# Kernel tuning notes

Hardware: AMD Instinct MI355X
Metric: run time of the kernel (lower is better)

Reference implementation:

```python
import jax, jax.numpy as jnp
import numpy as np

EPS = 1e-5

@jax.custom_vjp
def spike(u):
    return (u >= 0).astype(u.dtype)

def _spike_fwd(u):
    return spike(u), u

def _spike_bwd(u, g):
    return (g / (1.0 + 5.0 * jnp.abs(u)) ** 2,)

spike.defvjp(_spike_fwd, _spike_bwd)


def setup_inputs() -> dict:
    key = jax.random.key(0)
    ks = jax.random.split(key, 20)
    B, T, IN, TH, H = 2048, 320, 64, 128, 64
    d = {}
    d['x'] = jax.random.normal(ks[0], (B, T, IN), jnp.float32)
    d['tda'] = jax.random.normal(ks[1], (B, 150), jnp.float32)
    # depthwise conv: Conv1d(64,128,k=15,pad=7,groups=64) -> kernel [128, 1, 15]
    d['conv_w'] = jax.random.normal(ks[2], (TH, 1, 15), jnp.float32) * 0.1
    d['conv_b'] = jnp.zeros((TH,), jnp.float32)
    d['bn1_g'] = jnp.ones((TH,), jnp.float32)
    d['bn1_b'] = jnp.zeros((TH,), jnp.float32)
    d['bn1_m'] = jnp.zeros((TH,), jnp.float32)
    d['bn1_v'] = jnp.ones((TH,), jnp.float32)
    # spatial_fc: Linear(128,64), init mean=0.05 std=0.1
    d['sp_w'] = 0.05 + 0.1 * jax.random.normal(ks[3], (H, TH), jnp.float32)
    d['sp_b'] = jnp.zeros((H,), jnp.float32)
    d['li_w'] = jax.random.normal(ks[4], (H, 2 * H), jnp.float32) * (1.0 / np.sqrt(2 * H))
    d['li_b'] = jnp.zeros((H,), jnp.float32)
    d['tda_w1'] = jax.random.normal(ks[5], (64, 150), jnp.float32) * (1.0 / np.sqrt(150))
    d['tda_b1'] = jnp.zeros((64,), jnp.float32)
    d['tda_w2'] = jax.random.normal(ks[6], (32, 64), jnp.float32) * 0.125
    d['tda_b2'] = jnp.zeros((32,), jnp.float32)
    dp_out = (320 // 32) * H  # 640
    d['cls_w1'] = jax.random.normal(ks[7], (128, dp_out + 32), jnp.float32) * (1.0 / np.sqrt(dp_out + 32))
    d['cls_b1'] = jnp.zeros((128,), jnp.float32)
    d['bn2_g'] = jnp.ones((128,), jnp.float32)
    d['bn2_b'] = jnp.zeros((128,), jnp.float32)
    d['bn2_m'] = jnp.zeros((128,), jnp.float32)
    d['bn2_v'] = jnp.ones((128,), jnp.float32)
    d['cls_w2'] = jax.random.normal(ks[8], (4, 128), jnp.float32) * (1.0 / np.sqrt(128))
    d['cls_b2'] = jnp.zeros((4,), jnp.float32)
    return d


def reference(x, tda, conv_w, conv_b, bn1_g, bn1_b, bn1_m, bn1_v, sp_w, sp_b,
              li_w, li_b, tda_w1, tda_b1, tda_w2, tda_b2,
              cls_w1, cls_b1, bn2_g, bn2_b, bn2_m, bn2_v, cls_w2, cls_b2):
    B, T, _ = x.shape
    L_DP, N_DP, H = 32, 16, 64
    # temp_conv (eval mode: no dropout, BN with running stats)
    xc = jnp.transpose(x, (0, 2, 1))  # [B, 64, T]
    y = jax.lax.conv_general_dilated(
        xc, conv_w, window_strides=(1,), padding=[(7, 7)],
        dimension_numbers=('NCH', 'OIH', 'NCH'), feature_group_count=64)
    y = y + conv_b[None, :, None]
    y = (y - bn1_m[None, :, None]) * jax.lax.rsqrt(bn1_v + EPS)[None, :, None] * bn1_g[None, :, None] + bn1_b[None, :, None]
    y = jax.nn.relu(y)
    y = jnp.transpose(y, (0, 2, 1))  # [B, T, 128]
    # precompute all input currents: [T, B, 64] (time-major for scan)
    cur_all = jnp.einsum('bth,oh->tbo', y, sp_w) + sp_b

    def step(carry, cur):
        mf, ms, ml = carry
        mf = 0.5 * mf + cur
        sf = spike(mf - 0.5)
        mf = mf * (1.0 - sf)
        ms = 0.9 * ms + cur
        ss = spike(ms - 1.0)
        ms = ms * (1.0 - ss)
        cur_li = jnp.concatenate([sf, ss], axis=-1) @ li_w.T + li_b
        ml = 0.9 * ml + cur_li
        return (mf, ms, ml), ml

    z0 = jnp.zeros((B, H), x.dtype)
    _, li_seq = jax.lax.scan(step, (z0, z0, z0), cur_all)  # [T, B, 64]
    li_seq = jnp.transpose(li_seq, (1, 0, 2))  # [B, T, 64]

    windows = li_seq.reshape(B, T // L_DP, L_DP, H)
    start_mean = windows[:, :, :N_DP, :].mean(axis=2)
    end_mean = windows[:, :, -N_DP:, :].mean(axis=2)
    dp_feat = (end_mean - start_mean).reshape(B, -1)  # [B, 640]

    t1 = jax.nn.relu(tda @ tda_w1.T + tda_b1)
    tda_feat = jax.nn.relu(t1 @ tda_w2.T + tda_b2)  # [B, 32]

    h = jnp.concatenate([dp_feat, tda_feat], axis=-1) @ cls_w1.T + cls_b1
    h = (h - bn2_m) * jax.lax.rsqrt(bn2_v + EPS) * bn2_g + bn2_b
    h = jax.nn.relu(h)
    return h @ cls_w2.T + cls_b2  # [B, 4]
```

## Files before the change

kernel.cpp:

```cpp
#include <hip/hip_runtime.h>

#define NT 256

#define WS_SPWT    0
#define WS_SC1     8192
#define WS_SH1     8320
#define WS_SC2     8448
#define WS_SH2     8576
#define WS_LIWT    8704
#define WS_TW1T    16896
#define WS_TW2T    26496
#define WS_CW1T    28544
#define WS_TOTAL   114560
#define WS_WG      114560
#define WS_WBASE   114688

__global__ void prep_kernel(
    const float* __restrict__ conv_b, const float* __restrict__ bn1_g,
    const float* __restrict__ bn1_b,  const float* __restrict__ bn1_m,
    const float* __restrict__ bn1_v,  const float* __restrict__ sp_w,
    const float* __restrict__ li_w,   const float* __restrict__ tda_w1,
    const float* __restrict__ tda_w2, const float* __restrict__ cls_w1,
    const float* __restrict__ bn2_g,  const float* __restrict__ bn2_b,
    const float* __restrict__ bn2_m,  const float* __restrict__ bn2_v,
    float* __restrict__ ws)
{
    int i = blockIdx.x * NT + threadIdx.x;
    if (i > WS_TOTAL) return;
    if (i == WS_TOTAL) {
        float g = 0.f, sE = 0.f, sL = 0.f; int w = 0;
        for (int t = 0; t < 320; ++t) {
            g = fmaf(0.9f, g, 1.f);
            int pos = t & 31;
            if (pos < 16) sE += g; else sL += g;
            if (pos == 31) { ws[WS_WG + w] = sL - sE; ++w; sE = 0.f; sL = 0.f; }
        }
        return;
    }
    if (i < WS_SC1) {
        int c = i >> 6, h = i & 63;
        ws[i] = sp_w[h*128 + c];
    } else if (i < WS_SH1) {
        int c = i - WS_SC1;
        float vv = bn1_v[c] + 1e-5f;
        ws[i] = (float)((double)bn1_g[c] / sqrt((double)vv));
    } else if (i < WS_SC2) {
        int c = i - WS_SH1;
        float vv = bn1_v[c] + 1e-5f;
        double s = (double)bn1_g[c] / sqrt((double)vv);
        ws[i] = (float)(((double)conv_b[c] - (double)bn1_m[c])*s + (double)bn1_b[c]);
    } else if (i < WS_SH2) {
        int c = i - WS_SC2;
        float vv = bn2_v[c] + 1e-5f;
        ws[i] = (float)((double)bn2_g[c] / sqrt((double)vv));
    } else if (i < WS_LIWT) {
        int c = i - WS_SH2;
        float vv = bn2_v[c] + 1e-5f;
        double s = (double)bn2_g[c] / sqrt((double)vv);
        ws[i] = (float)((double)bn2_b[c] - (double)bn2_m[c]*s);
    } else if (i < WS_TW1T) {
        int t = i - WS_LIWT; int j = t >> 6, o = t & 63;
        ws[i] = li_w[o*128 + j];
    } else if (i < WS_TW2T) {
        int t = i - WS_TW1T; int r = t >> 6, o = t & 63;
        ws[i] = tda_w1[o*150 + r];
    } else if (i < WS_CW1T) {
        int t = i - WS_TW2T; int j = t >> 5, o = t & 31;
        ws[i] = tda_w2[o*64 + j];
    } else {
        int t = i - WS_CW1T; int j = t >> 7, c = t & 127;
        ws[i] = cls_w1[c*672 + j];
    }
}

__launch_bounds__(NT, 3)
__global__ void fused_kernel(
    const float* __restrict__ x, const float* __restrict__ conv_w,
    const float* __restrict__ sp_b, const float* __restrict__ ws,
    float* __restrict__ wfeat)
{
    __shared__ float y_lds[128*65];
    __shared__ float cur_lds[64*64];

    const int tid  = threadIdx.x;
    const int b    = blockIdx.x;
    const int ic   = tid & 63;
    const int tg   = tid >> 6;
    const int lane = tid & 63;
    const int h0   = __builtin_amdgcn_readfirstlane((tid >> 6) << 4);

    float w0[15], w1[15];
    #pragma unroll
    for (int k = 0; k < 15; ++k) {
        w0[k] = conv_w[(2*ic)*15 + k];
        w1[k] = conv_w[(2*ic + 1)*15 + k];
    }
    const float sA = ws[WS_SC1 + 2*ic],     hA = ws[WS_SH1 + 2*ic];
    const float sB = ws[WS_SC1 + 2*ic + 1], hB = ws[WS_SH1 + 2*ic + 1];
    const float4* bp = reinterpret_cast<const float4*>(sp_b + h0);
    const float4 b0v = bp[0], b1v = bp[1], b2v = bp[2], b3v = bp[3];

    const float* __restrict__ spwT = ws;
    const float* xb = x + (size_t)b * 20480 + ic;
    float* Wb = wfeat + (size_t)b * 1280;

    float mf = 0.f, ms = 0.f, rlo = 0.f, rhi = 0.f;

    float xr0[30], xr1[30];
    #pragma unroll
    for (int r = 0; r < 30; ++r) {
        int t = tg*16 - 7 + r;
        xr0[r] = (t >= 0) ? xb[(size_t)t * 64] : 0.f;
    }
    #pragma unroll
    for (int j = 0; j < 16; ++j) {
        float a0 = 0.f, a1 = 0.f;
        #pragma unroll
        for (int k = 0; k < 15; ++k) {
            a0 = fmaf(xr0[j + k], w0[k], a0);
            a1 = fmaf(xr0[j + k], w1[k], a1);
        }
        int tt = tg*16 + j;
        y_lds[(2*ic)*65 + tt]     = fmaxf(fmaf(a0, sA, hA), 0.f);
        y_lds[(2*ic + 1)*65 + tt] = fmaxf(fmaf(a1, sB, hB), 0.f);
    }
    __syncthreads();

    #pragma unroll
    for (int chk = 0; chk < 5; ++chk) {
        float* xn = (chk & 1) ? xr0 : xr1;

        if (chk < 4) {
            const int tbase = (chk + 1)*64 + tg*16 - 7;
            if (tbase + 29 < 320) {
                #pragma unroll
                for (int r = 0; r < 30; ++r)
                    xn[r] = xb[(size_t)(tbase + r) * 64];
            } else {
                #pragma unroll
                for (int r = 0; r < 30; ++r) {
                    int t = tbase + r;
                    xn[r] = (t < 320) ? xb[(size_t)t * 64] : 0.f;
                }
            }
        }

        {
            float acc[16];
            acc[0]=b0v.x;  acc[1]=b0v.y;  acc[2]=b0v.z;  acc[3]=b0v.w;
            acc[4]=b1v.x;  acc[5]=b1v.y;  acc[6]=b1v.z;  acc[7]=b1v.w;
            acc[8]=b2v.x;  acc[9]=b2v.y;  acc[10]=b2v.z; acc[11]=b2v.w;
            acc[12]=b3v.x; acc[13]=b3v.y; acc[14]=b3v.z; acc[15]=b3v.w;

            #pragma unroll 4
            for (int c = 0; c < 128; ++c) {
                float yv = y_lds[c*65 + lane];
                const float4* wp = reinterpret_cast<const float4*>(spwT + c*64 + h0);
                float4 q0 = wp[0], q1 = wp[1], q2 = wp[2], q3 = wp[3];
                acc[0]  = fmaf(yv, q0.x, acc[0]);
                acc[1]  = fmaf(yv, q0.y, acc[1]);
                acc[2]  = fmaf(yv, q0.z, acc[2]);
                acc[3]  = fmaf(yv, q0.w, acc[3]);
                acc[4]  = fmaf(yv, q1.x, acc[4]);
                acc[5]  = fmaf(yv, q1.y, acc[5]);
                acc[6]  = fmaf(yv, q1.z, acc[6]);
                acc[7]  = fmaf(yv, q1.w, acc[7]);
                acc[8]  = fmaf(yv, q2.x, acc[8]);
                acc[9]  = fmaf(yv, q2.y, acc[9]);
                acc[10] = fmaf(yv, q2.z, acc[10]);
                acc[11] = fmaf(yv, q2.w, acc[11]);
                acc[12] = fmaf(yv, q3.x, acc[12]);
                acc[13] = fmaf(yv, q3.y, acc[13]);
                acc[14] = fmaf(yv, q3.z, acc[14]);
                acc[15] = fmaf(yv, q3.w, acc[15]);
            }
            const int tsw = (lane & 15) << 2;
            #pragma unroll
            for (int k = 0; k < 4; ++k) {
                float4 v4 = make_float4(acc[4*k], acc[4*k+1], acc[4*k+2], acc[4*k+3]);
                *reinterpret_cast<float4*>(&cur_lds[lane*64 + ((h0 + 4*k) ^ tsw)]) = v4;
            }
        }
        __syncthreads();

        if (tid < 64) {
            float sE_lo = 0.f, sE_hi = 0.f;
            #pragma unroll
            for (int gq = 0; gq < 4; ++gq) {
                float v[16];
                #pragma unroll
                for (int q = 0; q < 16; ++q) {
                    int t = gq*16 + q;
                    v[q] = cur_lds[t*64 + (lane ^ ((t & 15) << 2))];
                }
                float slo = 0.f, shi = 0.f;
                #pragma unroll
                for (int q = 0; q < 16; ++q) {
                    float c = v[q];
                    mf = fmaf(0.5f, mf, c);
                    bool sf = mf >= 0.5f;
                    ms = fmaf(0.9f, ms, c);
                    bool ss = ms >= 1.0f;
                    mf = sf ? 0.f : mf;
                    ms = ss ? 0.f : ms;
                    rlo = fmaf(0.9f, rlo, sf ? 1.f : 0.f);
                    rhi = fmaf(0.9f, rhi, ss ? 1.f : 0.f);
                    slo += rlo; shi += rhi;
                }
                if ((gq & 1) == 0) {
                    sE_lo = slo; sE_hi = shi;
                } else {
                    int wdx = chk*2 + (gq >> 1);
                    Wb[wdx*128 + lane]      = slo - sE_lo;
                    Wb[wdx*128 + 64 + lane] = shi - sE_hi;
                }
            }
        }
        if (chk < 4) {
            #pragma unroll
            for (int j = 0; j < 16; ++j) {
                float a0 = 0.f, a1 = 0.f;
                #pragma unroll
                for (int k = 0; k < 15; ++k) {
                    a0 = fmaf(xn[j + k], w0[k], a0);
                    a1 = fmaf(xn[j + k], w1[k], a1);
                }
                int tt = tg*16 + j;
                y_lds[(2*ic)*65 + tt]     = fmaxf(fmaf(a0, sA, hA), 0.f);
                y_lds[(2*ic + 1)*65 + tt] = fmaxf(fmaf(a1, sB, hB), 0.f);
            }
        }
        __syncthreads();
    }
}

__global__ void epilogue_kernel(
    const float* __restrict__ tda,    const float* __restrict__ li_b,
    const float* __restrict__ tda_b1, const float* __restrict__ tda_b2,
    const float* __restrict__ cls_b1, const float* __restrict__ cls_w2,
    const float* __restrict__ cls_b2, const float* __restrict__ ws,
    const float* __restrict__ W,      float* __restrict__ out)
{
    __shared__ float Wl[1280];
    __shared__ float t1[64], tf[32], dp[640], h1[128];
    const int b = blockIdx.x, tid = threadIdx.x;

    for (int i = tid; i < 1280; i += NT)
        Wl[i] = W[(size_t)b*1280 + i];
    __syncthreads();

    const float* __restrict__ liwT = ws + WS_LIWT;
    const float* __restrict__ tw1T = ws + WS_TW1T;
    const float* __restrict__ tw2T = ws + WS_TW2T;
    const float* __restrict__ cw1T = ws + WS_CW1T;
    const float* tdab = tda + b*150;

    if (tid < 64) {
        float acc = tda_b1[tid];
        for (int i2 = 0; i2 < 150; ++i2)
            acc = fmaf(tdab[i2], tw1T[i2*64 + tid], acc);
        t1[tid] = fmaxf(acc, 0.f);
    }
    __syncthreads();
    if (tid < 32) {
        float acc = tda_b2[tid];
        #pragma unroll 8
        for (int j = 0; j < 64; ++j)
            acc = fmaf(t1[j], tw2T[j*32 + tid], acc);
        tf[tid] = fmaxf(acc, 0.f);
    }
    {
        int o = tid & 63;
        for (int w = tid >> 6; w < 10; w += 4) {
            float acc = li_b[o] * ws[WS_WG + w];
            #pragma unroll 4
            for (int j = 0; j < 128; ++j)
                acc = fmaf(Wl[w*128 + j], liwT[j*64 + o], acc);
            dp[w*64 + o] = 0.0625f * acc;
        }
    }
    __syncthreads();
    if (tid < 128) {
        float acc = cls_b1[tid];
        for (int j = 0; j < 640; ++j)
            acc = fmaf(dp[j], cw1T[j*128 + tid], acc);
        #pragma unroll 4
        for (int j = 0; j < 32; ++j)
            acc = fmaf(tf[j], cw1T[(640 + j)*128 + tid], acc);
        float s2 = ws[WS_SC2 + tid], sh2 = ws[WS_SH2 + tid];
        h1[tid] = fmaxf(fmaf(acc, s2, sh2), 0.f);
    }
    __syncthreads();
    if (tid < 4) {
        float acc = cls_b2[tid];
        for (int c = 0; c < 128; ++c)
            acc = fmaf(h1[c], cls_w2[tid*128 + c], acc);
        out[b*4 + tid] = acc;
    }
}

extern "C" void kernel_launch(void* const* d_in, const int* in_sizes, int n_in,
                              void* d_out, int out_size, void* d_ws, size_t ws_size,
                              hipStream_t stream) {
    const float* x      = (const float*)d_in[0];
    const float* tda    = (const float*)d_in[1];
    const float* conv_w = (const float*)d_in[2];
    const float* conv_b = (const float*)d_in[3];
    const float* bn1_g  = (const float*)d_in[4];
    const float* bn1_b  = (const float*)d_in[5];
    const float* bn1_m  = (const float*)d_in[6];
    const float* bn1_v  = (const float*)d_in[7];
    const float* sp_w   = (const float*)d_in[8];
    const float* sp_b   = (const float*)d_in[9];
    const float* li_w   = (const float*)d_in[10];
    const float* li_b   = (const float*)d_in[11];
    const float* tda_w1 = (const float*)d_in[12];
    const float* tda_b1 = (const float*)d_in[13];
    const float* tda_w2 = (const float*)d_in[14];
    const float* tda_b2 = (const float*)d_in[15];
    const float* cls_w1 = (const float*)d_in[16];
    const float* cls_b1 = (const float*)d_in[17];
    const float* bn2_g  = (const float*)d_in[18];
    const float* bn2_b  = (const float*)d_in[19];
    const float* bn2_m  = (const float*)d_in[20];
    const float* bn2_v  = (const float*)d_in[21];
    const float* cls_w2 = (const float*)d_in[22];
    const float* cls_b2 = (const float*)d_in[23];
    float* ws  = (float*)d_ws;
    float* out = (float*)d_out;

    const int B = in_sizes[0] / (320 * 64);

    prep_kernel<<<(WS_TOTAL + 1 + NT - 1)/NT, NT, 0, stream>>>(
        conv_b, bn1_g, bn1_b, bn1_m, bn1_v, sp_w,
        li_w, tda_w1, tda_w2, cls_w1,
        bn2_g, bn2_b, bn2_m, bn2_v, ws);

    fused_kernel<<<B, NT, 0, stream>>>(
        x, conv_w, sp_b, ws, ws + WS_WBASE);

    epilogue_kernel<<<B, NT, 0, stream>>>(
        tda, li_b, tda_b1, tda_b2, cls_b1, cls_w2, cls_b2,
        ws, ws + WS_WBASE, out);
}
```

Baseline: 249.7 us.

## Fuse epilogue into main kernel and rotate scan wave across chunks

Moves the classifier/TDA epilogue into the tail of the fused kernel, which removes a separate launch and reuses the shared-memory buffers. The sequential LIF scan now runs on a different wave each chunk, with its state passed through LDS, so the serial work is spread across SIMDs. The TDA first layer is computed by an otherwise idle wave during the last chunk. The costs are extra LDS traffic for the state and longer per-block tail work, which may affect occupancy.

```diff
diff --git a/kernel.cpp b/kernel.cpp
--- a/kernel.cpp
+++ b/kernel.cpp
@@ -75,18 +75,25 @@
 
 __launch_bounds__(NT, 3)
 __global__ void fused_kernel(
-    const float* __restrict__ x, const float* __restrict__ conv_w,
-    const float* __restrict__ sp_b, const float* __restrict__ ws,
-    float* __restrict__ wfeat)
+    const float* __restrict__ x,      const float* __restrict__ conv_w,
+    const float* __restrict__ sp_b,   const float* __restrict__ tda,
+    const float* __restrict__ li_b,   const float* __restrict__ tda_b1,
+    const float* __restrict__ tda_b2, const float* __restrict__ cls_b1,
+    const float* __restrict__ cls_w2, const float* __restrict__ cls_b2,
+    const float* __restrict__ ws,     float* __restrict__ wfeat,
+    float* __restrict__ out)
 {
     __shared__ float y_lds[128*65];
     __shared__ float cur_lds[64*64];
+    __shared__ float st_lds[4*64];
+    __shared__ float t1_lds[64];
 
     const int tid  = threadIdx.x;
     const int b    = blockIdx.x;
     const int ic   = tid & 63;
     const int tg   = tid >> 6;
     const int lane = tid & 63;
+    const int wid  = tid >> 6;
     const int h0   = __builtin_amdgcn_readfirstlane((tid >> 6) << 4);
 
     float w0[15], w1[15];
@@ -103,8 +110,6 @@
     const float* __restrict__ spwT = ws;
     const float* xb = x + (size_t)b * 20480 + ic;
     float* Wb = wfeat + (size_t)b * 1280;
-
-    float mf = 0.f, ms = 0.f, rlo = 0.f, rhi = 0.f;
 
     float xr0[30], xr1[30];
     #pragma unroll
@@ -183,7 +188,16 @@
         }
         __syncthreads();
 
-        if (tid < 64) {
+        if (wid == (chk & 3)) {
+            float mf, ms, rlo, rhi;
+            if (chk == 0) {
+                mf = 0.f; ms = 0.f; rlo = 0.f; rhi = 0.f;
+            } else {
+                mf  = st_lds[0*64 + lane];
+                ms  = st_lds[1*64 + lane];
+                rlo = st_lds[2*64 + lane];
+                rhi = st_lds[3*64 + lane];
+            }
             float sE_lo = 0.f, sE_hi = 0.f;
             #pragma unroll
             for (int gq = 0; gq < 4; ++gq) {
@@ -215,7 +229,21 @@
                     Wb[wdx*128 + 64 + lane] = shi - sE_hi;
                 }
             }
-        }
+            if (chk < 4) {
+                st_lds[0*64 + lane] = mf;
+                st_lds[1*64 + lane] = ms;
+                st_lds[2*64 + lane] = rlo;
+                st_lds[3*64 + lane] = rhi;
+            }
+        } else if (chk == 4 && wid == 1) {
+            const float* tdab = tda + (size_t)b * 150;
+            const float* __restrict__ tw1T = ws + WS_TW1T;
+            float acc = tda_b1[lane];
+            for (int i2 = 0; i2 < 150; ++i2)
+                acc = fmaf(tdab[i2], tw1T[i2*64 + lane], acc);
+            t1_lds[lane] = fmaxf(acc, 0.f);
+        }
+
         if (chk < 4) {
             #pragma unroll
             for (int j = 0; j < 16; ++j) {
@@ -232,43 +260,25 @@
         }
         __syncthreads();
     }
-}
-
-__global__ void epilogue_kernel(
-    const float* __restrict__ tda,    const float* __restrict__ li_b,
-    const float* __restrict__ tda_b1, const float* __restrict__ tda_b2,
-    const float* __restrict__ cls_b1, const float* __restrict__ cls_w2,
-    const float* __restrict__ cls_b2, const float* __restrict__ ws,
-    const float* __restrict__ W,      float* __restrict__ out)
-{
-    __shared__ float Wl[1280];
-    __shared__ float t1[64], tf[32], dp[640], h1[128];
-    const int b = blockIdx.x, tid = threadIdx.x;
-
-    for (int i = tid; i < 1280; i += NT)
-        Wl[i] = W[(size_t)b*1280 + i];
-    __syncthreads();
-
+
+    float* Wl = cur_lds;
+    float* tf = cur_lds + 1280;
+    float* dp = cur_lds + 1312;
+    float* h1 = cur_lds + 1952;
     const float* __restrict__ liwT = ws + WS_LIWT;
-    const float* __restrict__ tw1T = ws + WS_TW1T;
     const float* __restrict__ tw2T = ws + WS_TW2T;
     const float* __restrict__ cw1T = ws + WS_CW1T;
-    const float* tdab = tda + b*150;
-
-    if (tid < 64) {
-        float acc = tda_b1[tid];
-        for (int i2 = 0; i2 < 150; ++i2)
-            acc = fmaf(tdab[i2], tw1T[i2*64 + tid], acc);
-        t1[tid] = fmaxf(acc, 0.f);
-    }
-    __syncthreads();
+
+    for (int i = tid; i < 1280; i += NT)
+        Wl[i] = Wb[i];
     if (tid < 32) {
         float acc = tda_b2[tid];
         #pragma unroll 8
         for (int j = 0; j < 64; ++j)
-            acc = fmaf(t1[j], tw2T[j*32 + tid], acc);
+            acc = fmaf(t1_lds[j], tw2T[j*32 + tid], acc);
         tf[tid] = fmaxf(acc, 0.f);
     }
+    __syncthreads();
     {
         int o = tid & 63;
         for (int w = tid >> 6; w < 10; w += 4) {
@@ -295,7 +305,7 @@
         float acc = cls_b2[tid];
         for (int c = 0; c < 128; ++c)
             acc = fmaf(h1[c], cls_w2[tid*128 + c], acc);
-        out[b*4 + tid] = acc;
+        out[(size_t)b*4 + tid] = acc;
     }
 }
 
@@ -337,9 +347,6 @@
         bn2_g, bn2_b, bn2_m, bn2_v, ws);
 
     fused_kernel<<<B, NT, 0, stream>>>(
-        x, conv_w, sp_b, ws, ws + WS_WBASE);
-
-    epilogue_kernel<<<B, NT, 0, stream>>>(
-        tda, li_b, tda_b1, tda_b2, cls_b1, cls_w2, cls_b2,
-        ws, ws + WS_WBASE, out);
+        x, conv_w, sp_b, tda, li_b, tda_b1, tda_b2,
+        cls_b1, cls_w2, cls_b2, ws, ws + WS_WBASE, out);
 }
```

New measurement: 365.1 us. +46.2%, slower.
